# Optimization experiments

Hardware: AMD Instinct MI355X
Metric: run time of the kernel (lower is better)

The kernel has to match this reference:

```python
import jax, jax.numpy as jnp
import numpy as np

PADDING_BORDER = True   # padding_mode=True -> border padding
ALIGN_CORNERS = True


def setup_inputs() -> dict:
    key = jax.random.key(0)
    k1, k2 = jax.random.split(key)
    N, C, L_in, L_out = 64, 64, 4096, 8192
    inp = jax.random.normal(k1, (N, C, L_in), dtype=jnp.float32)
    grid = jax.random.uniform(k2, (N, L_out), dtype=jnp.float32) * 2.0 - 1.0  # [-1, 1]
    return {"input": inp, "grid": grid}


def _grid_sample1d(inp, grid, padding_border, align_corners):
    N, C, L = inp.shape
    # unnormalize grid coord from [-1,1] to pixel space
    if align_corners:
        x = (grid + 1.0) * 0.5 * (L - 1)
    else:
        x = ((grid + 1.0) * L - 1.0) * 0.5
    if padding_border:
        x = jnp.clip(x, 0.0, float(L - 1))
    x0 = jnp.floor(x)
    w1 = x - x0          # weight for right neighbor, [N, L_out]
    w0 = 1.0 - w1        # weight for left neighbor
    i0 = x0.astype(jnp.int32)
    i1 = i0 + 1
    if padding_border:
        m0 = jnp.ones_like(w0)
        m1 = jnp.ones_like(w1)
    else:
        m0 = ((i0 >= 0) & (i0 < L)).astype(inp.dtype)
        m1 = ((i1 >= 0) & (i1 < L)).astype(inp.dtype)
    i0c = jnp.clip(i0, 0, L - 1)
    i1c = jnp.clip(i1, 0, L - 1)
    # gather along length dim: indices broadcast over channels -> [N, C, L_out]
    v0 = jnp.take_along_axis(inp, i0c[:, None, :].repeat(1, axis=1), axis=2)
    v1 = jnp.take_along_axis(inp, i1c[:, None, :].repeat(1, axis=1), axis=2)
    out = (w0 * m0)[:, None, :] * v0 + (w1 * m1)[:, None, :] * v1
    return out


def reference(input, grid):
    return _grid_sample1d(input, grid, PADDING_BORDER, ALIGN_CORNERS)
```

## Files before the change

kernel.cpp:

```cpp
#include <hip/hip_runtime.h>


constexpr int N_    = 64;
constexpr int C_    = 64;
constexpr int L_IN  = 4096;
constexpr int L_OUT = 8192;

constexpr int BLOCK   = 1024;
constexpr int C_LDS   = 4;
constexpr int NCHUNK  = C_ / C_LDS;
constexpr int NBLOCKS = N_ * NCHUNK;

__global__ __launch_bounds__(BLOCK, 8) void gs1d_kernel(
    const float* __restrict__ inp, const float* __restrict__ grid,
    float* __restrict__ out)
{
    __shared__ float lds[C_LDS * L_IN];

    const int tid = threadIdx.x;
    const int bid = blockIdx.x;
    const int n   = bid >> 4;
    const int cc  = bid & (NCHUNK - 1);

    const float* src = inp + ((size_t)n * C_ + (size_t)cc * C_LDS) * L_IN;

#pragma unroll
    for (int k = 0; k < 4; ++k) {
        int e     = (k * BLOCK + tid) * 4;
        int lbase = (k * BLOCK + (tid & ~63)) * 4;
        __builtin_amdgcn_global_load_lds(
            (const __attribute__((address_space(1))) void*)(src + e),
            (__attribute__((address_space(3))) void*)(&lds[lbase]),
            16, 0, 0);
    }

    const float* grow = grid + (size_t)n * L_OUT;
    float4 g0 = *reinterpret_cast<const float4*>(grow + 4 * tid);
    float4 g1 = *reinterpret_cast<const float4*>(grow + L_OUT / 2 + 4 * tid);

    float gv[8] = {g0.x, g0.y, g0.z, g0.w, g1.x, g1.y, g1.z, g1.w};
    int   li[8];
    float w1[8];
#pragma unroll
    for (int j = 0; j < 8; ++j) {
        float x = (gv[j] + 1.0f) * 0.5f * (float)(L_IN - 1);
        x = fminf(fmaxf(x, 0.0f), (float)(L_IN - 1));
        float xf = floorf(x);
        int   i0 = (int)xf;
        float w  = x - xf;
        li[j] = min(i0, L_IN - 2);
        w1[j] = (i0 >= L_IN - 1) ? 1.0f : w;
    }

    __syncthreads();

    float* out_base = out + ((size_t)n * C_ + (size_t)cc * C_LDS) * L_OUT;

#pragma unroll
    for (int c = 0; c < C_LDS; ++c) {
        const float* row = &lds[c * L_IN];
#pragma unroll
        for (int h = 0; h < 2; ++h) {
            float4 o;
            float* op = &o.x;
#pragma unroll
            for (int j = 0; j < 4; ++j) {
                int   p = h * 4 + j;
                float a = row[li[p]];
                float b = row[li[p] + 1];
                op[j] = fmaf(w1[p], b - a, a);
            }
            *reinterpret_cast<float4*>(
                out_base + (size_t)c * L_OUT + h * (L_OUT / 2) + 4 * tid) = o;
        }
    }
}

extern "C" void kernel_launch(void* const* d_in, const int* in_sizes, int n_in,
                              void* d_out, int out_size, void* d_ws, size_t ws_size,
                              hipStream_t stream) {
    const float* inp  = (const float*)d_in[0];
    const float* grid = (const float*)d_in[1];
    float* out = (float*)d_out;
    gs1d_kernel<<<NBLOCKS, BLOCK, 0, stream>>>(inp, grid, out);
}
```

Before: 185.4 us.

## Switch to one block per (n,c) row with 256 threads and nontemporal stores

Each block now handles a single input row (16KB LDS) with 256 threads, looping over eight output chunks. Grid coordinates and interpolation weights are recomputed per channel rather than amortized across four channels. Outputs are written with nontemporal stores to avoid polluting cache. The grid loads for the first half are issued before the barrier to overlap with the LDS fill. This trades grid reuse and extra index arithmetic for smaller blocks, more blocks in flight, and higher occupancy.

```diff
diff --git a/kernel.cpp b/kernel.cpp
--- a/kernel.cpp
+++ b/kernel.cpp
@@ -6,72 +6,66 @@
 constexpr int L_IN  = 4096;
 constexpr int L_OUT = 8192;
 
-constexpr int BLOCK   = 1024;
-constexpr int C_LDS   = 4;
-constexpr int NCHUNK  = C_ / C_LDS;
-constexpr int NBLOCKS = N_ * NCHUNK;
+constexpr int BLOCK  = 256;
+constexpr int CHUNKS = L_OUT / (BLOCK * 4);
+constexpr int NBLOCKS = N_ * C_;
+
+typedef float f32x4 __attribute__((ext_vector_type(4)));
 
 __global__ __launch_bounds__(BLOCK, 8) void gs1d_kernel(
     const float* __restrict__ inp, const float* __restrict__ grid,
     float* __restrict__ out)
 {
-    __shared__ float lds[C_LDS * L_IN];
+    __shared__ float row[L_IN];
 
     const int tid = threadIdx.x;
     const int bid = blockIdx.x;
-    const int n   = bid >> 4;
-    const int cc  = bid & (NCHUNK - 1);
+    const int n   = bid >> 6;
 
-    const float* src = inp + ((size_t)n * C_ + (size_t)cc * C_LDS) * L_IN;
-
+    const float* src = inp + (size_t)bid * L_IN;
 #pragma unroll
     for (int k = 0; k < 4; ++k) {
         int e     = (k * BLOCK + tid) * 4;
         int lbase = (k * BLOCK + (tid & ~63)) * 4;
         __builtin_amdgcn_global_load_lds(
             (const __attribute__((address_space(1))) void*)(src + e),
-            (__attribute__((address_space(3))) void*)(&lds[lbase]),
+            (__attribute__((address_space(3))) void*)(&row[lbase]),
             16, 0, 0);
     }
 
     const float* grow = grid + (size_t)n * L_OUT;
-    float4 g0 = *reinterpret_cast<const float4*>(grow + 4 * tid);
-    float4 g1 = *reinterpret_cast<const float4*>(grow + L_OUT / 2 + 4 * tid);
-
-    float gv[8] = {g0.x, g0.y, g0.z, g0.w, g1.x, g1.y, g1.z, g1.w};
-    int   li[8];
-    float w1[8];
-#pragma unroll
-    for (int j = 0; j < 8; ++j) {
-        float x = (gv[j] + 1.0f) * 0.5f * (float)(L_IN - 1);
-        x = fminf(fmaxf(x, 0.0f), (float)(L_IN - 1));
-        float xf = floorf(x);
-        int   i0 = (int)xf;
-        float w  = x - xf;
-        li[j] = min(i0, L_IN - 2);
-        w1[j] = (i0 >= L_IN - 1) ? 1.0f : w;
-    }
-
-    __syncthreads();
-
-    float* out_base = out + ((size_t)n * C_ + (size_t)cc * C_LDS) * L_OUT;
+    float*       orow = out  + (size_t)bid * L_OUT;
 
 #pragma unroll
-    for (int c = 0; c < C_LDS; ++c) {
-        const float* row = &lds[c * L_IN];
+    for (int half = 0; half < 2; ++half) {
+        float4 g[4];
 #pragma unroll
-        for (int h = 0; h < 2; ++h) {
-            float4 o;
-            float* op = &o.x;
+        for (int h = 0; h < 4; ++h)
+            g[h] = *reinterpret_cast<const float4*>(
+                grow + (half * 4 + h) * (BLOCK * 4) + 4 * tid);
+
+        if (half == 0) __syncthreads();
+
+#pragma unroll
+        for (int h = 0; h < 4; ++h) {
+            const float* gp = &g[h].x;
+            f32x4 o;
 #pragma unroll
             for (int j = 0; j < 4; ++j) {
-                int   p = h * 4 + j;
-                float a = row[li[p]];
-                float b = row[li[p] + 1];
-                op[j] = fmaf(w1[p], b - a, a);
+                float x = (gp[j] + 1.0f) * 0.5f * (float)(L_IN - 1);
+                x = fminf(fmaxf(x, 0.0f), (float)(L_IN - 1));
+                float xf = floorf(x);
+                int   i0 = (int)xf;
+                float w  = x - xf;
+                int   li = min(i0, L_IN - 2);
+                float w1 = (i0 >= L_IN - 1) ? 1.0f : w;
+                float a = row[li];
+                float b = row[li + 1];
+                o[j] = fmaf(w1, b - a, a);
             }
-            *reinterpret_cast<float4*>(
-                out_base + (size_t)c * L_OUT + h * (L_OUT / 2) + 4 * tid) = o;
+            __builtin_nontemporal_store(o,
+                reinterpret_cast<f32x4*>(
+                    orow + (half * 4 + h) * (BLOCK * 4) + 4 * tid));
         }
     }
 }
```

Result: no change. 183.7 us (-0.9%).
